# Kernel optimization log

Hardware: AMD Instinct MI355X
Metric: run time of the kernel (lower is better)

## Reference

```python
import jax, jax.numpy as jnp
import numpy as np

NFFT = 4096
BATCH = 2048
STAGES = 12  # log2(NFFT)


def _bitrev(n):
    bits = int(np.log2(n))
    idx = np.arange(n)
    rev = np.zeros(n, dtype=np.int64)
    for b in range(bits):
        rev |= ((idx >> b) & 1) << (bits - 1 - b)
    return rev


def setup_inputs() -> dict:
    key = jax.random.key(0)
    x = jax.random.normal(key, (BATCH, NFFT), dtype=jnp.float32)
    # bit-reversal permutation matrix, applied as x @ perm -> x[bitrev(k)]
    rev = _bitrev(NFFT)
    perm = np.zeros((NFFT, NFFT), dtype=np.float32)
    perm[rev, np.arange(NFFT)] = 1.0
    # per-stage butterfly weights (real/imag of twiddles), zero-padded to NFFT
    rconvs = np.zeros((STAGES, 2, NFFT), dtype=np.float32)
    iconvs = np.zeros((STAGES, 2, NFFT), dtype=np.float32)
    for i in range(STAGES):
        s = 2 ** (i + 1)
        h = 2 ** i
        th = 2.0 * np.pi * np.arange(h) / s  # twiddle w^j = exp(-i*th)
        c, sn = np.cos(th), np.sin(th)
        rconvs[i, 0, :s] = 1.0
        rconvs[i, 1, :s] = np.concatenate([c, -c])
        iconvs[i, 1, :s] = np.concatenate([-sn, sn])
    return {
        "x": x,
        "perm": jnp.asarray(perm),
        "rconvs": jnp.asarray(rconvs),
        "iconvs": jnp.asarray(iconvs),
    }


def _butterfly(x, w, h):
    # x: [B, M, 2h], w: [2, 2h]; equals the original diag-filter conv1d
    xt, xb = x[..., :h], x[..., h:]
    top = w[0, :h] * xt + w[1, :h] * xb
    bot = w[0, h:] * xt + w[1, h:] * xb
    return jnp.concatenate([top, bot], axis=-1)


def reference(x, perm, rconvs, iconvs):
    B = x.shape[0]
    rx = x @ perm  # bit-reversal reorder (dense matmul as in original)
    ix = jnp.zeros_like(rx)
    for i in range(STAGES):
        s = 2 ** (i + 1)
        h = 2 ** i
        rx = rx.reshape(B, -1, s)
        ix = ix.reshape(B, -1, s)
        rc = rconvs[i, :, :s]
        ic = iconvs[i, :, :s]
        nrx = _butterfly(rx, rc, h) - _butterfly(ix, ic, h)
        nix = _butterfly(ix, rc, h) + _butterfly(rx, ic, h)
        rx = nrx.reshape(B, -1)
        ix = nix.reshape(B, -1)
    return rx.reshape(B, 1, NFFT), ix.reshape(B, 1, NFFT)
```

## Files before the change

### kernel.cpp

```cpp
#include <hip/hip_runtime.h>


constexpr int NFFT  = 4096;
constexpr int BATCH = 2048;
constexpr int QN    = NFFT / 4;
constexpr float TWOPI_OVER_N = 6.28318530717958647692f / (float)NFFT;

__global__ __launch_bounds__(1024)
void fft4096_r4(const float* __restrict__ x, float* __restrict__ out) {
    __shared__ __align__(16) float sAre[NFFT];
    __shared__ __align__(16) float sAim[NFFT];
    __shared__ __align__(16) float sBre[NFFT];
    __shared__ __align__(16) float sBim[NFFT];

    const int row = blockIdx.x;
    const int t   = threadIdx.x;
    const float* __restrict__ xr = x + (size_t)row * NFFT;

    {
        float a = xr[t];
        float b = xr[t + QN];
        float c = xr[t + 2 * QN];
        float d = xr[t + 3 * QN];
        float t0 = a + c, t1 = a - c, t2 = b + d, t3 = b - d;
        float B1r = t1, B1i = -t3;
        float B3r = t1, B3i = t3;
        float alpha = TWOPI_OVER_N * (float)t;
        float s1, c1;
        __sincosf(alpha, &s1, &c1);
        float c2 = c1 * c1 - s1 * s1, s2 = 2.0f * s1 * c1;
        float c3 = c1 * c2 - s1 * s2, s3 = s1 * c2 + c1 * s2;
        float4 re4, im4;
        re4.x = t0 + t2;              im4.x = 0.0f;
        re4.y = B1r * c1 + B1i * s1;  im4.y = B1i * c1 - B1r * s1;
        re4.z = (t0 - t2) * c2;       im4.z = -(t0 - t2) * s2;
        re4.w = B3r * c3 + B3i * s3;  im4.w = B3i * c3 - B3r * s3;
        reinterpret_cast<float4*>(sAre)[t] = re4;
        reinterpret_cast<float4*>(sAim)[t] = im4;
    }

    float* srcRe = sAre; float* srcIm = sAim;
    float* dstRe = sBre; float* dstIm = sBim;
#pragma unroll
    for (int st = 1; st <= 4; ++st) {
        __syncthreads();
        const int s = 1 << (2 * st);
        const int q = t & (s - 1);
        const int f = t - q;
        float ar = srcRe[t],          ai = srcIm[t];
        float br = srcRe[t + QN],     bi = srcIm[t + QN];
        float cr = srcRe[t + 2 * QN], ci = srcIm[t + 2 * QN];
        float dr = srcRe[t + 3 * QN], di = srcIm[t + 3 * QN];
        float t0r = ar + cr, t0i = ai + ci;
        float t1r = ar - cr, t1i = ai - ci;
        float t2r = br + dr, t2i = bi + di;
        float t3r = bi - di, t3i = dr - br;
        float B0r = t0r + t2r, B0i = t0i + t2i;
        float B1r = t1r + t3r, B1i = t1i + t3i;
        float B2r = t0r - t2r, B2i = t0i - t2i;
        float B3r = t1r - t3r, B3i = t1i - t3i;
        float alpha = TWOPI_OVER_N * (float)f;
        float s1, c1;
        __sincosf(alpha, &s1, &c1);
        float c2 = c1 * c1 - s1 * s1, s2 = 2.0f * s1 * c1;
        float c3 = c1 * c2 - s1 * s2, s3 = s1 * c2 + c1 * s2;
        const int base = 4 * t - 3 * q;
        dstRe[base]         = B0r;                 dstIm[base]         = B0i;
        dstRe[base + s]     = B1r * c1 + B1i * s1; dstIm[base + s]     = B1i * c1 - B1r * s1;
        dstRe[base + 2 * s] = B2r * c2 + B2i * s2; dstIm[base + 2 * s] = B2i * c2 - B2r * s2;
        dstRe[base + 3 * s] = B3r * c3 + B3i * s3; dstIm[base + 3 * s] = B3i * c3 - B3r * s3;
        float* tr = srcRe; srcRe = dstRe; dstRe = tr;
        float* ti = srcIm; srcIm = dstIm; dstIm = ti;
    }

    __syncthreads();
    {
        float ar = srcRe[t],          ai = srcIm[t];
        float br = srcRe[t + QN],     bi = srcIm[t + QN];
        float cr = srcRe[t + 2 * QN], ci = srcIm[t + 2 * QN];
        float dr = srcRe[t + 3 * QN], di = srcIm[t + 3 * QN];
        float t0r = ar + cr, t0i = ai + ci;
        float t1r = ar - cr, t1i = ai - ci;
        float t2r = br + dr, t2i = bi + di;
        float t3r = bi - di, t3i = dr - br;
        float* __restrict__ outRe = out + (size_t)row * NFFT;
        float* __restrict__ outIm = out + (size_t)BATCH * NFFT + (size_t)row * NFFT;
        outRe[t]          = t0r + t2r;  outIm[t]          = t0i + t2i;
        outRe[t + QN]     = t1r + t3r;  outIm[t + QN]     = t1i + t3i;
        outRe[t + 2 * QN] = t0r - t2r;  outIm[t + 2 * QN] = t0i - t2i;
        outRe[t + 3 * QN] = t1r - t3r;  outIm[t + 3 * QN] = t1i - t3i;
    }
}

extern "C" void kernel_launch(void* const* d_in, const int* in_sizes, int n_in,
                              void* d_out, int out_size, void* d_ws, size_t ws_size,
                              hipStream_t stream) {
    (void)in_sizes; (void)n_in; (void)d_ws; (void)ws_size; (void)out_size;
    const float* x = (const float*)d_in[0];
    float* out = (float*)d_out;
    fft4096_r4<<<dim3(BATCH), dim3(1024), 0, stream>>>(x, out);
}
```

Before: 133.5 us.

## Replace radix-4 six-pass FFT with three-pass radix-16 register FFT

Restructures the 4096-point FFT from six radix-4 passes on 1024 threads into three radix-16 passes on 256 threads, each holding 16 complex values in registers. Shared memory becomes one padded float2 buffer (row stride 18) instead of four ping-pong arrays, and the number of barriers and shared-memory round trips drops from five to three. Twiddles are built from one sin/cos per thread by repeated complex multiplication. The cost is much higher register pressure per thread and possible accuracy drift from the chained twiddle products.

After: 132.6 us (median of 2 runs). About the same (-0.7%).

```diff
diff --git a/kernel.cpp b/kernel.cpp
--- a/kernel.cpp
+++ b/kernel.cpp
@@ -3,92 +3,112 @@
 
 constexpr int NFFT  = 4096;
 constexpr int BATCH = 2048;
-constexpr int QN    = NFFT / 4;
-constexpr float TWOPI_OVER_N = 6.28318530717958647692f / (float)NFFT;
+constexpr int RS    = 18;
 
-__global__ __launch_bounds__(1024)
-void fft4096_r4(const float* __restrict__ x, float* __restrict__ out) {
-    __shared__ __align__(16) float sAre[NFFT];
-    __shared__ __align__(16) float sAim[NFFT];
-    __shared__ __align__(16) float sBre[NFFT];
-    __shared__ __align__(16) float sBim[NFFT];
+struct cplx { float re, im; };
+__device__ __forceinline__ cplx cmul(cplx a, cplx b){ return {a.re*b.re - a.im*b.im, a.re*b.im + a.im*b.re}; }
+__device__ __forceinline__ cplx cadd(cplx a, cplx b){ return {a.re+b.re, a.im+b.im}; }
+__device__ __forceinline__ cplx csub(cplx a, cplx b){ return {a.re-b.re, a.im-b.im}; }
+__device__ __forceinline__ cplx cnegi(cplx a){ return { a.im, -a.re }; }
+
+__device__ __forceinline__ void dft4(cplx& a, cplx& b, cplx& c, cplx& d){
+    cplx t0 = cadd(a,c), t1 = csub(a,c), t2 = cadd(b,d);
+    cplx t3n = cnegi(csub(b,d));
+    a = cadd(t0,t2);
+    cplx nb = cadd(t1,t3n);
+    c = csub(t0,t2);
+    d = csub(t1,t3n);
+    b = nb;
+}
+
+__device__ __forceinline__ constexpr int RIDX(int r){ return 4*(r&3) + (r>>2); }
+
+__device__ __forceinline__ void dft16(cplx z[16]){
+    dft4(z[0], z[4], z[8],  z[12]);
+    dft4(z[1], z[5], z[9],  z[13]);
+    dft4(z[2], z[6], z[10], z[14]);
+    dft4(z[3], z[7], z[11], z[15]);
+    constexpr float C1 = 0.92387953251128675613f;
+    constexpr float S1 = 0.38268343236508977173f;
+    constexpr float R2 = 0.70710678118654752440f;
+    z[5]  = cmul(z[5],  { C1,-S1});
+    z[6]  = cmul(z[6],  { R2,-R2});
+    z[7]  = cmul(z[7],  { S1,-C1});
+    z[9]  = cmul(z[9],  { R2,-R2});
+    z[10] = cnegi(z[10]);
+    z[11] = cmul(z[11], {-R2,-R2});
+    z[13] = cmul(z[13], { S1,-C1});
+    z[14] = cmul(z[14], {-R2,-R2});
+    z[15] = cmul(z[15], {-C1, S1});
+    dft4(z[0],  z[1],  z[2],  z[3]);
+    dft4(z[4],  z[5],  z[6],  z[7]);
+    dft4(z[8],  z[9],  z[10], z[11]);
+    dft4(z[12], z[13], z[14], z[15]);
+}
+
+__device__ __forceinline__ void twiddle_all(cplx z[16], float rev){
+    float ang = rev * 6.28318530717958647692f;
+    float s = __sinf(ang), c = __cosf(ang);
+    cplx w[16];
+    w[0] = {1.0f, 0.0f};
+    w[1] = {c, -s};
+#pragma unroll
+    for (int r = 2; r < 16; ++r) w[r] = cmul(w[r>>1], w[(r+1)>>1]);
+#pragma unroll
+    for (int r = 1; r < 16; ++r) z[RIDX(r)] = cmul(z[RIDX(r)], w[r]);
+}
+
+__global__ __launch_bounds__(256, 4)
+void fft4096_r16(const float* __restrict__ x, float* __restrict__ out) {
+    __shared__ float2 su[256 * RS];
 
     const int row = blockIdx.x;
     const int t   = threadIdx.x;
     const float* __restrict__ xr = x + (size_t)row * NFFT;
 
+    cplx z[16];
+
+#pragma unroll
+    for (int n1 = 0; n1 < 16; ++n1) z[n1] = { xr[n1*256 + t], 0.0f };
+    dft16(z);
+    twiddle_all(z, (float)t * (1.0f/4096.0f));
+#pragma unroll
+    for (int r = 0; r < 16; ++r) su[t*RS + r] = { z[RIDX(r)].re, z[RIDX(r)].im };
+
+    __syncthreads();
+
     {
-        float a = xr[t];
-        float b = xr[t + QN];
-        float c = xr[t + 2 * QN];
-        float d = xr[t + 3 * QN];
-        float t0 = a + c, t1 = a - c, t2 = b + d, t3 = b - d;
-        float B1r = t1, B1i = -t3;
-        float B3r = t1, B3i = t3;
-        float alpha = TWOPI_OVER_N * (float)t;
-        float s1, c1;
-        __sincosf(alpha, &s1, &c1);
-        float c2 = c1 * c1 - s1 * s1, s2 = 2.0f * s1 * c1;
-        float c3 = c1 * c2 - s1 * s2, s3 = s1 * c2 + c1 * s2;
-        float4 re4, im4;
-        re4.x = t0 + t2;              im4.x = 0.0f;
-        re4.y = B1r * c1 + B1i * s1;  im4.y = B1i * c1 - B1r * s1;
-        re4.z = (t0 - t2) * c2;       im4.z = -(t0 - t2) * s2;
-        re4.w = B3r * c3 + B3i * s3;  im4.w = B3i * c3 - B3r * s3;
-        reinterpret_cast<float4*>(sAre)[t] = re4;
-        reinterpret_cast<float4*>(sAim)[t] = im4;
-    }
-
-    float* srcRe = sAre; float* srcIm = sAim;
-    float* dstRe = sBre; float* dstIm = sBim;
+        const int k1 = t >> 4, m2 = t & 15;
 #pragma unroll
-    for (int st = 1; st <= 4; ++st) {
+        for (int m1 = 0; m1 < 16; ++m1) {
+            float2 v = su[(16*m1 + m2)*RS + k1];
+            z[m1] = { v.x, v.y };
+        }
+        dft16(z);
+        twiddle_all(z, (float)m2 * (1.0f/256.0f));
         __syncthreads();
-        const int s = 1 << (2 * st);
-        const int q = t & (s - 1);
-        const int f = t - q;
-        float ar = srcRe[t],          ai = srcIm[t];
-        float br = srcRe[t + QN],     bi = srcIm[t + QN];
-        float cr = srcRe[t + 2 * QN], ci = srcIm[t + 2 * QN];
-        float dr = srcRe[t + 3 * QN], di = srcIm[t + 3 * QN];
-        float t0r = ar + cr, t0i = ai + ci;
-        float t1r = ar - cr, t1i = ai - ci;
-        float t2r = br + dr, t2i = bi + di;
-        float t3r = bi - di, t3i = dr - br;
-        float B0r = t0r + t2r, B0i = t0i + t2i;
-        float B1r = t1r + t3r, B1i = t1i + t3i;
-        float B2r = t0r - t2r, B2i = t0i - t2i;
-        float B3r = t1r - t3r, B3i = t1i - t3i;
-        float alpha = TWOPI_OVER_N * (float)f;
-        float s1, c1;
-        __sincosf(alpha, &s1, &c1);
-        float c2 = c1 * c1 - s1 * s1, s2 = 2.0f * s1 * c1;
-        float c3 = c1 * c2 - s1 * s2, s3 = s1 * c2 + c1 * s2;
-        const int base = 4 * t - 3 * q;
-        dstRe[base]         = B0r;                 dstIm[base]         = B0i;
-        dstRe[base + s]     = B1r * c1 + B1i * s1; dstIm[base + s]     = B1i * c1 - B1r * s1;
-        dstRe[base + 2 * s] = B2r * c2 + B2i * s2; dstIm[base + 2 * s] = B2i * c2 - B2r * s2;
-        dstRe[base + 3 * s] = B3r * c3 + B3i * s3; dstIm[base + 3 * s] = B3i * c3 - B3r * s3;
-        float* tr = srcRe; srcRe = dstRe; dstRe = tr;
-        float* ti = srcIm; srcIm = dstIm; dstIm = ti;
+#pragma unroll
+        for (int k2 = 0; k2 < 16; ++k2)
+            su[(k1*16 + k2)*RS + m2] = { z[RIDX(k2)].re, z[RIDX(k2)].im };
     }
 
     __syncthreads();
+
     {
-        float ar = srcRe[t],          ai = srcIm[t];
-        float br = srcRe[t + QN],     bi = srcIm[t + QN];
-        float cr = srcRe[t + 2 * QN], ci = srcIm[t + 2 * QN];
-        float dr = srcRe[t + 3 * QN], di = srcIm[t + 3 * QN];
-        float t0r = ar + cr, t0i = ai + ci;
-        float t1r = ar - cr, t1i = ai - ci;
-        float t2r = br + dr, t2i = bi + di;
-        float t3r = bi - di, t3i = dr - br;
+        const int k1 = t & 15, k2 = t >> 4;
+#pragma unroll
+        for (int m2 = 0; m2 < 16; ++m2) {
+            float2 v = su[(k1*16 + k2)*RS + m2];
+            z[m2] = { v.x, v.y };
+        }
+        dft16(z);
         float* __restrict__ outRe = out + (size_t)row * NFFT;
         float* __restrict__ outIm = out + (size_t)BATCH * NFFT + (size_t)row * NFFT;
-        outRe[t]          = t0r + t2r;  outIm[t]          = t0i + t2i;
-        outRe[t + QN]     = t1r + t3r;  outIm[t + QN]     = t1i + t3i;
-        outRe[t + 2 * QN] = t0r - t2r;  outIm[t + 2 * QN] = t0i - t2i;
-        outRe[t + 3 * QN] = t1r - t3r;  outIm[t + 3 * QN] = t1i - t3i;
+#pragma unroll
+        for (int k3 = 0; k3 < 16; ++k3) {
+            outRe[t + 256*k3] = z[RIDX(k3)].re;
+            outIm[t + 256*k3] = z[RIDX(k3)].im;
+        }
     }
 }
 
@@ -98,5 +118,5 @@
     (void)in_sizes; (void)n_in; (void)d_ws; (void)ws_size; (void)out_size;
     const float* x = (const float*)d_in[0];
     float* out = (float*)d_out;
-    fft4096_r4<<<dim3(BATCH), dim3(1024), 0, stream>>>(x, out);
+    fft4096_r16<<<dim3(BATCH), dim3(256), 0, stream>>>(x, out);
 }
```
